# Kernel tuning notes

Hardware: AMD Instinct MI355X
Metric: run time of the kernel (lower is better)

Reference implementation:

```python
import jax, jax.numpy as jnp
import numpy as np
from jax import lax

B, IN_C, H, W = 2, 256, 80, 80
OUT_C = 256
INTER = IN_C // 16          # 16
C4 = IN_C // 4              # 64
K = 3
DIL = [7, 5, 2, 1]
PADS = [(K + (K - 1) * (d - 1)) // 2 for d in DIL]  # same-padding per module formula


def conv2d(x, w, b=None, pad=0, dil=1, groups=1):
    out = lax.conv_general_dilated(
        x, w, (1, 1), [(pad, pad), (pad, pad)], rhs_dilation=(dil, dil),
        dimension_numbers=('NCHW', 'OIHW', 'NCHW'), feature_group_count=groups)
    if b is not None:
        out = out + b[None, :, None, None]
    return out


def bnorm(x, g, b, eps=1e-3):
    # BatchNorm2d in training mode (fresh module): biased batch stats, eps=0.001
    m = x.mean((0, 2, 3), keepdims=True)
    v = x.var((0, 2, 3), keepdims=True)
    return (x - m) * lax.rsqrt(v + eps) * g[None, :, None, None] + b[None, :, None, None]


def gnorm(x, g, b, groups=4, eps=1e-5):
    Bb, C, Hh, Ww = x.shape
    xr = x.reshape(Bb, groups, C // groups, Hh, Ww)
    m = xr.mean((2, 3, 4), keepdims=True)
    v = xr.var((2, 3, 4), keepdims=True)
    xr = (xr - m) * lax.rsqrt(v + eps)
    return xr.reshape(Bb, C, Hh, Ww) * g[None, :, None, None] + b[None, :, None, None]


def setup_inputs() -> dict:
    keys = jax.random.split(jax.random.key(0), 40)

    def w_init(k, shape):
        fan = float(np.prod(shape[1:]))
        return jax.random.normal(k, shape, jnp.float32) / np.sqrt(fan)

    d = {}
    d['z'] = jax.random.normal(keys[0], (B, IN_C, H, W), jnp.float32)
    for i in range(4):  # depthwise dilated convs: (C4, 1, 3, 3)
        d[f'w_at{i}'] = w_init(keys[1 + 2 * i], (C4, 1, K, K))
        d[f'b_at{i}'] = jax.random.normal(keys[2 + 2 * i], (C4,), jnp.float32) * 0.02
    d['gn_w'] = 1.0 + 0.05 * jax.random.normal(keys[9], (IN_C,), jnp.float32)
    d['gn_b'] = 0.05 * jax.random.normal(keys[10], (IN_C,), jnp.float32)
    d['conv_w'] = w_init(keys[11], (IN_C, IN_C, 1, 1))
    d['conv_b'] = jax.random.normal(keys[12], (IN_C,), jnp.float32) * 0.02
    d['c5a_w'] = w_init(keys[13], (INTER, IN_C, 3, 3))
    d['bn5a_w'] = 1.0 + 0.05 * jax.random.normal(keys[14], (INTER,), jnp.float32)
    d['bn5a_b'] = 0.05 * jax.random.normal(keys[15], (INTER,), jnp.float32)
    d['c5c_w'] = w_init(keys[16], (INTER, IN_C, 3, 3))
    d['bn5c_w'] = 1.0 + 0.05 * jax.random.normal(keys[17], (INTER,), jnp.float32)
    d['bn5c_b'] = 0.05 * jax.random.normal(keys[18], (INTER,), jnp.float32)
    d['pq_w'] = w_init(keys[19], (INTER // 8, INTER, 1, 1))
    d['pq_b'] = jax.random.normal(keys[20], (INTER // 8,), jnp.float32) * 0.02
    d['pk_w'] = w_init(keys[21], (INTER // 8, INTER, 1, 1))
    d['pk_b'] = jax.random.normal(keys[22], (INTER // 8,), jnp.float32) * 0.02
    d['pv_w'] = w_init(keys[23], (INTER, INTER, 1, 1))
    d['pv_b'] = jax.random.normal(keys[24], (INTER,), jnp.float32) * 0.02
    d['pa_gamma'] = 0.5 * jnp.ones((1,), jnp.float32)  # nonzero so attn path is exercised
    d['ca_gamma'] = 0.5 * jnp.ones((1,), jnp.float32)
    d['c5b_w'] = w_init(keys[25], (INTER, INTER, 3, 3))
    d['bn5b_w'] = 1.0 + 0.05 * jax.random.normal(keys[26], (INTER,), jnp.float32)
    d['bn5b_b'] = 0.05 * jax.random.normal(keys[27], (INTER,), jnp.float32)
    d['c5d_w'] = w_init(keys[28], (INTER, INTER, 3, 3))
    d['bn5d_w'] = 1.0 + 0.05 * jax.random.normal(keys[29], (INTER,), jnp.float32)
    d['bn5d_b'] = 0.05 * jax.random.normal(keys[30], (INTER,), jnp.float32)
    d['c6_w'] = w_init(keys[31], (OUT_C, INTER, 1, 1))
    d['c6_b'] = jax.random.normal(keys[32], (OUT_C,), jnp.float32) * 0.02
    return d


def reference(z, w_at0, b_at0, w_at1, b_at1, w_at2, b_at2, w_at3, b_at3,
              gn_w, gn_b, conv_w, conv_b,
              c5a_w, bn5a_w, bn5a_b, c5c_w, bn5c_w, bn5c_b,
              pq_w, pq_b, pk_w, pk_b, pv_w, pv_b, pa_gamma, ca_gamma,
              c5b_w, bn5b_w, bn5b_b, c5d_w, bn5d_w, bn5d_b, c6_w, c6_b):
    parts = jnp.split(z, 4, axis=1)
    ws = [w_at0, w_at1, w_at2, w_at3]
    bs = [b_at0, b_at1, b_at2, b_at3]
    zs = [conv2d(parts[i], ws[i], bs[i], pad=PADS[i], dil=DIL[i], groups=C4)
          for i in range(4)]
    zc = jnp.concatenate(zs, axis=1)
    zc = jax.nn.gelu(conv2d(gnorm(zc, gn_w, gn_b), conv_w, conv_b), approximate=False)

    # --- DABlock ---
    feat1 = jax.nn.relu(bnorm(conv2d(zc, c5a_w, pad=1), bn5a_w, bn5a_b))
    Bb, C, Hh, Ww = feat1.shape
    N = Hh * Ww
    # PAM: full HWxHW attention
    q = conv2d(feat1, pq_w, pq_b).reshape(Bb, -1, N)   # (B, C//8, N)
    k = conv2d(feat1, pk_w, pk_b).reshape(Bb, -1, N)
    v = conv2d(feat1, pv_w, pv_b).reshape(Bb, C, N)
    energy = jnp.einsum('bcn,bcm->bnm', q, k)          # (B, N, N)
    att = jax.nn.softmax(energy, axis=-1)
    pa = jnp.einsum('bcm,bnm->bcn', v, att).reshape(Bb, C, Hh, Ww)
    pa = pa_gamma * pa + feat1
    pa_conv = jax.nn.relu(bnorm(conv2d(pa, c5b_w, pad=1), bn5b_w, bn5b_b))

    feat2 = jax.nn.relu(bnorm(conv2d(zc, c5c_w, pad=1), bn5c_w, bn5c_b))
    # CAM: CxC attention
    xf = feat2.reshape(Bb, C, N)
    e = jnp.einsum('bcn,bdn->bcd', xf, xf)             # (B, C, C)
    e = e.max(-1, keepdims=True) - e
    att_c = jax.nn.softmax(e, axis=-1)
    ca = jnp.einsum('bcd,bdn->bcn', att_c, xf).reshape(Bb, C, Hh, Ww)
    ca = ca_gamma * ca + feat2
    ca_conv = jax.nn.relu(bnorm(conv2d(ca, c5d_w, pad=1), bn5d_w, bn5d_b))

    # Dropout2d(p=0.05) is identity in eval mode
    out = jax.nn.relu(conv2d(pa_conv + ca_conv, c6_w, c6_b))
    return out
```

## Files before the change

kernel.cpp:

```cpp
#include <hip/hip_runtime.h>
#include <math.h>

#define HW 6400

typedef __attribute__((ext_vector_type(8))) short bf16x8;
typedef __attribute__((ext_vector_type(4))) float f32x4;

__device__ __forceinline__ float wredsum(float v){
  #pragma unroll
  for (int o = 32; o; o >>= 1) v += __shfl_xor(v, o);
  return v;
}

__device__ __forceinline__ unsigned short f2bf(float f){
  unsigned int u = __float_as_uint(f);
  u += 0x7FFF + ((u >> 16) & 1);
  return (unsigned short)(u >> 16);
}

__device__ __forceinline__ float bf2f(unsigned short s){
  return __uint_as_float((unsigned int)s << 16);
}

__device__ __forceinline__ unsigned int cvt_pk_bf16(float lo, float hi){
  unsigned int r;
  asm("v_cvt_pk_bf16_f32 %0, %1, %2" : "=v"(r) : "v"(lo), "v"(hi));
  return r;
}

__device__ __forceinline__ float gelu(float v){
  return 0.5f * v * (1.f + erff(v * 0.70710678118f));
}

__global__ __launch_bounds__(256) void k_prep(
    const float* __restrict__ wa, const float* __restrict__ wc,
    const float* __restrict__ wb, const float* __restrict__ wd,
    const float* __restrict__ cw, const float* __restrict__ gn_sc,
    const float* __restrict__ cb,
    unsigned short* __restrict__ wbbf,
    unsigned short* __restrict__ cwbf, float* __restrict__ cbp,
    unsigned short* __restrict__ wbbf2){
  int bx = blockIdx.x;
  int tid = threadIdx.x;
  if (bx < 288){
    int i = bx * 256 + tid;
    if (i < 73728){
      int j = i & 7, l = (i >> 3) & 63, f = (i >> 9) & 1, ss = i >> 10;
      int k = ss * 32 + (l >> 4) * 8 + j;
      int off = k >> 8, ic = k & 255;
      int oc = f * 16 + (l & 15);
      float v = (oc < 16) ? wa[(oc * 256 + ic) * 9 + off]
                          : wc[((oc - 16) * 256 + ic) * 9 + off];
      wbbf[i] = f2bf(v);
    }
  } else if (bx < 800){
    int i = (bx - 288) * 256 + tid;
    int b = i >> 16, r = i & 65535;
    int j = r & 7, l = (r >> 3) & 63, f = (r >> 9) & 15, ss = r >> 13;
    int ic = ss * 32 + (l >> 4) * 8 + j;
    int oc = f * 16 + (l & 15);
    cwbf[i] = f2bf(cw[oc * 256 + ic] * gn_sc[(b * 256 + ic) * 2]);
  } else if (bx < 832){
    int bb = bx - 800;
    int b = bb >> 4;
    int oc = (bb & 15) * 16 + (tid >> 4);
    int cp = tid & 15;
    float s2 = 0.f;
    #pragma unroll
    for (int k = 0; k < 16; k++){
      int c = cp * 16 + k;
      s2 += cw[oc * 256 + c] * gn_sc[(b * 256 + c) * 2 + 1];
    }
    s2 += __shfl_xor(s2, 1); s2 += __shfl_xor(s2, 2);
    s2 += __shfl_xor(s2, 4); s2 += __shfl_xor(s2, 8);
    if (cp == 0) cbp[b * 256 + oc] = cb[oc] + s2;
  } else {
    int i = (bx - 832) * 256 + tid;
    if (i < 9216){
      int j = i & 7, l = (i >> 3) & 63, f = (i >> 9) & 1, off = i >> 10;
      int kk = (l >> 4) * 8 + j;
      int oc = f * 16 + (l & 15);
      float v = 0.f;
      if (oc < 16 && kk < 16)        v = wb[(oc * 16 + kk) * 9 + off];
      else if (oc >= 16 && kk >= 16) v = wd[((oc - 16) * 16 + (kk - 16)) * 9 + off];
      wbbf2[i] = f2bf(v);
    }
  }
}

__global__ __launch_bounds__(256) void k_dwt(
    const float* __restrict__ z,
    const float* __restrict__ w0, const float* __restrict__ b0,
    const float* __restrict__ w1, const float* __restrict__ b1,
    const float* __restrict__ w2, const float* __restrict__ b2,
    const float* __restrict__ w3, const float* __restrict__ b3,
    unsigned short* __restrict__ zbf, float* __restrict__ gnpart){
  __shared__ unsigned short lt[64][66];
  int tid = threadIdx.x;
  int g = blockIdx.y, b = blockIdx.z;
  int p0 = blockIdx.x * 64;
  int lane = tid & 63, s = tid >> 6;
  int pix = p0 + lane;
  int h = pix / 80, w = pix % 80;
  const float* wp; const float* bp; int d;
  if (g == 0){ wp = w0; bp = b0; d = 7; }
  else if (g == 1){ wp = w1; bp = b1; d = 5; }
  else if (g == 2){ wp = w2; bp = b2; d = 2; }
  else            { wp = w3; bp = b3; d = 1; }
  int offr[9]; float msk[9];
  #pragma unroll
  for (int kh = 0; kh < 3; kh++){
    #pragma unroll
    for (int kw = 0; kw < 3; kw++){
      bool ok = ((unsigned)(h + (kh - 1) * d) < 80u) && ((unsigned)(w + (kw - 1) * d) < 80u);
      offr[kh * 3 + kw] = ok ? ((kh - 1) * d * 80 + (kw - 1) * d) : 0;
      msk[kh * 3 + kw] = ok ? 1.f : 0.f;
    }
  }
  const float* zb = z + (size_t)(b * 256 + g * 64) * HW + pix;
  for (int j = 0; j < 16; j++){
    int cl = s * 16 + j;
    const float* zin = zb + (size_t)cl * HW;
    const float* wr = wp + cl * 9;
    float acc = bp[cl];
    #pragma unroll
    for (int k = 0; k < 9; k++) acc = fmaf(wr[k], zin[offr[k]] * msk[k], acc);
    float S = wredsum(acc), Q = wredsum(acc * acc);
    if (lane == 0){
      int cg = b * 256 + g * 64 + cl;
      gnpart[(cg * 100 + blockIdx.x) * 2]     = S;
      gnpart[(cg * 100 + blockIdx.x) * 2 + 1] = Q;
    }
    lt[lane][cl] = f2bf(acc);
  }
  __syncthreads();
  int pr = tid >> 2, q = tid & 3;
  const unsigned short* src = &lt[pr][q * 16];
  unsigned int tmp[8];
  #pragma unroll
  for (int u = 0; u < 8; u++) tmp[u] = *(const unsigned int*)(src + u * 2);
  uint4 v0 = make_uint4(tmp[0], tmp[1], tmp[2], tmp[3]);
  uint4 v1 = make_uint4(tmp[4], tmp[5], tmp[6], tmp[7]);
  unsigned short* dst = zbf + ((size_t)b * HW + p0 + pr) * 256 + g * 64 + q * 16;
  *(uint4*)dst = v0;
  *(uint4*)(dst + 8) = v1;
}

__global__ __launch_bounds__(256) void k_gnfin(
    const float* __restrict__ gnpart, const float* __restrict__ gn_w,
    const float* __restrict__ gn_b, float* __restrict__ gn_sc){
  int tid = threadIdx.x; int bg = blockIdx.x;
  int b = bg >> 2, g = bg & 3;
  size_t base = (size_t)(b * 256 + g * 64) * 200;
  float S = 0.f, Q = 0.f;
  for (int i = tid; i < 6400; i += 256){
    S += gnpart[base + 2 * i];
    Q += gnpart[base + 2 * i + 1];
  }
  S = wredsum(S); Q = wredsum(Q);
  __shared__ float l[8];
  int lane = tid & 63, wid = tid >> 6;
  if (lane == 0){ l[wid] = S; l[4 + wid] = Q; }
  __syncthreads();
  float SS = l[0] + l[1] + l[2] + l[3];
  float QQ = l[4] + l[5] + l[6] + l[7];
  float M = 64.f * HW;
  float mean = SS / M;
  float var = QQ / M - mean * mean;
  float rstd = rsqrtf(var + 1e-5f);
  if (tid < 64){
    int c = g * 64 + tid;
    float sc = gn_w[c] * rstd;
    float sh = gn_b[c] - mean * sc;
    gn_sc[(b * 256 + c) * 2] = sc;
    gn_sc[(b * 256 + c) * 2 + 1] = sh;
  }
}

__global__ __launch_bounds__(256) void k_conv1_mfma(
    const unsigned short* __restrict__ zbf,
    const unsigned short* __restrict__ cwbf,
    const float* __restrict__ cbp,
    unsigned short* __restrict__ zbfT){
  __shared__ __align__(16) unsigned char lmem[64 * 512];
  unsigned short* lda = (unsigned short*)lmem;
  unsigned short* lout = (unsigned short*)lmem;
  int tid = threadIdx.x;
  int p0 = blockIdx.x * 64, ocg = blockIdx.y, b = blockIdx.z;
  #pragma unroll
  for (int k = 0; k < 8; k++){
    int m = tid + k * 256;
    int i = m >> 5, c = m & 31;
    bf16x8 val = *(const bf16x8*)(zbf + ((size_t)b * HW + p0 + i) * 256 + c * 8);
    *(bf16x8*)(lda + i * 256 + (c ^ (i & 7)) * 8) = val;
  }
  __syncthreads();
  int wv = tid >> 6, l = tid & 63;
  int row = l & 15, kg = l >> 4;
  int i = wv * 16 + row;
  f32x4 acc0 = {0.f,0.f,0.f,0.f}, acc1 = {0.f,0.f,0.f,0.f};
  f32x4 acc2 = {0.f,0.f,0.f,0.f}, acc3 = {0.f,0.f,0.f,0.f};
  const unsigned short* wp = cwbf + (size_t)b * 65536 + (ocg * 4) * 512 + l * 8;
  #pragma unroll
  for (int s = 0; s < 8; s++){
    int c = s * 4 + kg;
    bf16x8 a = *(const bf16x8*)(lda + i * 256 + (c ^ (i & 7)) * 8);
    const unsigned short* wps = wp + s * 8192;
    bf16x8 b0 = *(const bf16x8*)(wps);
    bf16x8 b1 = *(const bf16x8*)(wps + 512);
    bf16x8 b2 = *(const bf16x8*)(wps + 1024);
    bf16x8 b3 = *(const bf16x8*)(wps + 1536);
    acc0 = __builtin_amdgcn_mfma_f32_16x16x32_bf16(a, b0, acc0, 0, 0, 0);
    acc1 = __builtin_amdgcn_mfma_f32_16x16x32_bf16(a, b1, acc1, 0, 0, 0);
    acc2 = __builtin_amdgcn_mfma_f32_16x16x32_bf16(a, b2, acc2, 0, 0, 0);
    acc3 = __builtin_amdgcn_mfma_f32_16x16x32_bf16(a, b3, acc3, 0, 0, 0);
  }
  __syncthreads();
  const float* cbb = cbp + b * 256 + ocg * 64;
  int oc_l = l & 15;
  int pl = wv * 16 + kg * 4;
  float bs0 = cbb[oc_l], bs1 = cbb[16 + oc_l], bs2 = cbb[32 + oc_l], bs3 = cbb[48 + oc_l];
  #pragma unroll
  for (int r = 0; r < 4; r++){
    lout[(pl + r) * 72 + oc_l]      = f2bf(gelu(acc0[r] + bs0));
    lout[(pl + r) * 72 + 16 + oc_l] = f2bf(gelu(acc1[r] + bs1));
    lout[(pl + r) * 72 + 32 + oc_l] = f2bf(gelu(acc2[r] + bs2));
    lout[(pl + r) * 72 + 48 + oc_l] = f2bf(gelu(acc3[r] + bs3));
  }
  __syncthreads();
  int pix = tid >> 2, q = tid & 3;
  unsigned short* dst = zbfT + ((size_t)b * HW + p0 + pix) * 256 + ocg * 64 + q * 16;
  const unsigned short* src = lout + pix * 72 + q * 16;
  *(uint4*)dst       = *(const uint4*)src;
  *(uint4*)(dst + 8) = *(const uint4*)(src + 8);
}

__device__ __forceinline__ void c5_gload(bf16x8* r, const unsigned short* zbase,
    int p0, int irow, int c31, const int* hh, const int* ww, int off){
  int dy = off / 3 - 1, dx = off % 3 - 1;
  int doff = dy * 80 + dx;
  #pragma unroll
  for (int k = 0; k < 8; k++){
    int op = p0 + irow + k * 8;
    bool v = ((unsigned)(hh[k] + dy) < 80u) && ((unsigned)(ww[k] + dx) < 80u);
    int sp = v ? (op + doff) : op;
    bf16x8 val = *(const bf16x8*)(zbase + (size_t)sp * 256 + c31 * 8);
    if (!v) val = (bf16x8){0, 0, 0, 0, 0, 0, 0, 0};
    r[k] = val;
  }
}

__global__ __launch_bounds__(256) void k_conv5ac2(
    const unsigned short* __restrict__ zbfT,
    const unsigned short* __restrict__ wbbf,
    float* __restrict__ fpre, float* __restrict__ bnpart){
  __shared__ __align__(16) unsigned short lda[64 * 256];
  int tid = threadIdx.x;
  int och = blockIdx.y, b = blockIdx.z;
  int p0 = blockIdx.x * 64;
  int irow = tid >> 5, c31 = tid & 31;
  int hh[8], ww[8];
  #pragma unroll
  for (int k = 0; k < 8; k++){
    int op = p0 + irow + k * 8;
    hh[k] = op / 80; ww[k] = op % 80;
  }
  const unsigned short* zbase = zbfT + (size_t)b * HW * 256;
  bf16x8 r[8];
  c5_gload(r, zbase, p0, irow, c31, hh, ww, 0);
  #pragma unroll
  for (int k = 0; k < 8; k++){
    int i = irow + k * 8;
    *(bf16x8*)(lda + i * 256 + (c31 ^ (i & 7)) * 8) = r[k];
  }
  c5_gload(r, zbase, p0, irow, c31, hh, ww, 1);
  int wv = tid >> 6, l = tid & 63;
  int lrow = l & 15, kg = l >> 4;
  int li = wv * 16 + lrow;
  f32x4 acc = {0.f, 0.f, 0.f, 0.f};
  for (int off = 0; off < 9; off++){
    __syncthreads();
    const unsigned short* wp = wbbf + (size_t)off * 8192 + och * 512 + l * 8;
    #pragma unroll
    for (int s = 0; s < 8; s++){
      int cc = s * 4 + kg;
      bf16x8 a = *(const bf16x8*)(lda + li * 256 + (cc ^ (li & 7)) * 8);
      bf16x8 bb = *(const bf16x8*)(wp + s * 1024);
      acc = __builtin_amdgcn_mfma_f32_16x16x32_bf16(a, bb, acc, 0, 0, 0);
    }
    if (off + 1 < 9){
      __syncthreads();
      #pragma unroll
      for (int k = 0; k < 8; k++){
        int i = irow + k * 8;
        *(bf16x8*)(lda + i * 256 + (c31 ^ (i & 7)) * 8) = r[k];
      }
      if (off + 2 < 9) c5_gload(r, zbase, p0, irow, c31, hh, ww, off + 2);
    }
  }
  __syncthreads();
  float* lout = (float*)lda;
  int ocl = l & 15;
  int pl = wv * 16 + kg * 4;
  #pragma unroll
  for (int rr = 0; rr < 4; rr++) lout[ocl * 68 + pl + rr] = acc[rr];
  __syncthreads();
  int oc = tid >> 4, px = (tid & 15) * 4;
  float4 v = *(float4*)(lout + oc * 68 + px);
  *(float4*)(fpre + ((size_t)(b * 32 + och * 16 + oc)) * HW + p0 + px) = v;
  float S = v.x + v.y + v.z + v.w;
  float Q = v.x * v.x + v.y * v.y + v.z * v.z + v.w * v.w;
  #pragma unroll
  for (int o2 = 1; o2 < 16; o2 <<= 1){ S += __shfl_xor(S, o2); Q += __shfl_xor(Q, o2); }
  if ((tid & 15) == 0){
    int ocg = och * 16 + oc;
    bnpart[ocg * 400 + (b * 100 + blockIdx.x) * 2]     = S;
    bnpart[ocg * 400 + (b * 100 + blockIdx.x) * 2 + 1] = Q;
  }
}

__global__ __launch_bounds__(256) void k_featqkv(
    const float* __restrict__ fpre, const float* __restrict__ bnpart,
    const float* __restrict__ w1, const float* __restrict__ b1,
    const float* __restrict__ w2, const float* __restrict__ b2,
    const float* __restrict__ pqw, const float* __restrict__ pqb,
    const float* __restrict__ pkw, const float* __restrict__ pkb,
    const float* __restrict__ pvw, const float* __restrict__ pvb,
    float* __restrict__ feat, float* __restrict__ qkvT){
  __shared__ float lS[8][32], lQ[8][32], lsc[64];
  int tid = threadIdx.x; int b = blockIdx.y;
  {
    int oc = tid & 31, sl = tid >> 5;
    float S = 0.f, Q = 0.f;
    for (int i = sl; i < 200; i += 8){
      S += bnpart[oc * 400 + i * 2];
      Q += bnpart[oc * 400 + i * 2 + 1];
    }
    lS[sl][oc] = S; lQ[sl][oc] = Q;
    __syncthreads();
    if (tid < 32){
      float SS = 0.f, QQ = 0.f;
      #pragma unroll
      for (int s = 0; s < 8; s++){ SS += lS[s][tid]; QQ += lQ[s][tid]; }
      float M = 2.f * HW;
      float mean = SS / M, var = QQ / M - mean * mean;
      float rstd = rsqrtf(var + 1e-3f);
      float w  = (tid < 16) ? w1[tid] : w2[tid - 16];
      float bb = (tid < 16) ? b1[tid] : b2[tid - 16];
      float sc = w * rstd;
      lsc[tid * 2] = sc; lsc[tid * 2 + 1] = bb - mean * sc;
    }
    __syncthreads();
  }
  int n = blockIdx.x * 256 + tid;
  float f1[16], f2[16];
  #pragma unroll
  for (int c = 0; c < 16; c++){
    float v1 = fpre[(b * 32 + c) * HW + n] * lsc[c * 2] + lsc[c * 2 + 1];
    f1[c] = fmaxf(v1, 0.f);
    float v2 = fpre[(b * 32 + 16 + c) * HW + n] * lsc[(16 + c) * 2] + lsc[(16 + c) * 2 + 1];
    f2[c] = fmaxf(v2, 0.f);
    feat[(b * 32 + c) * HW + n] = f1[c];
    feat[(b * 32 + 16 + c) * HW + n] = f2[c];
  }
  float* o = qkvT + ((size_t)b * HW + n) * 20;
  #pragma unroll
  for (int j = 0; j < 2; j++){
    float q = pqb[j], k = pkb[j];
    #pragma unroll
    for (int c = 0; c < 16; c++){ q += pqw[j * 16 + c] * f1[c]; k += pkw[j * 16 + c] * f1[c]; }
    o[j] = q; o[2 + j] = k;
  }
  #pragma unroll
  for (int j = 0; j < 16; j++){
    float v = pvb[j];
    #pragma unroll
    for (int c = 0; c < 16; c++) v += pvw[j * 16 + c] * f1[c];
    o[4 + j] = v;
  }
}

__global__ __launch_bounds__(256) void k_pam_a(
    const float* __restrict__ qkvT, float* __restrict__ part){
  __shared__ __align__(16) float lk0[800];
  __shared__ __align__(16) float lk1[800];
  __shared__ __align__(16) unsigned short lvb[16][808];
  __shared__ float lred[4];
  int tid = threadIdx.x;
  int mc = blockIdx.y, b = blockIdx.z;
  float sqm = 0.f;
  for (int m = tid; m < 800; m += 256){
    const float* kv = qkvT + ((size_t)b * HW + mc * 800 + m) * 20;
    float4 a0 = *(const float4*)kv;
    lk0[m] = a0.z; lk1[m] = a0.w;
    sqm = fmaxf(sqm, a0.z * a0.z + a0.w * a0.w);
    float4 v0 = *(const float4*)(kv + 4);
    float4 v1 = *(const float4*)(kv + 8);
    float4 v2 = *(const float4*)(kv + 12);
    float4 v3 = *(const float4*)(kv + 16);
    lvb[0][m]  = f2bf(v0.x); lvb[1][m]  = f2bf(v0.y);
    lvb[2][m]  = f2bf(v0.z); lvb[3][m]  = f2bf(v0.w);
    lvb[4][m]  = f2bf(v1.x); lvb[5][m]  = f2bf(v1.y);
    lvb[6][m]  = f2bf(v1.z); lvb[7][m]  = f2bf(v1.w);
    lvb[8][m]  = f2bf(v2.x); lvb[9][m]  = f2bf(v2.y);
    lvb[10][m] = f2bf(v2.z); lvb[11][m] = f2bf(v2.w);
    lvb[12][m] = f2bf(v3.x); lvb[13][m] = f2bf(v3.y);
    lvb[14][m] = f2bf(v3.z); lvb[15][m] = f2bf(v3.w);
  }
  #pragma unroll
  for (int o = 32; o; o >>= 1) sqm = fmaxf(sqm, __shfl_xor(sqm, o));
  int lane = tid & 63, wid = tid >> 6;
  if (lane == 0) lred[wid] = sqm;
  __syncthreads();
  float kmax = sqrtf(fmaxf(fmaxf(lred[0], lred[1]), fmaxf(lred[2], lred[3])));
  int wv = tid >> 6, l = tid & 63;
  int row = l & 15, kg = l >> 4;
  int n = blockIdx.x * 64 + wv * 16 + row;
  const float* qp = qkvT + ((size_t)b * HW + n) * 20;
  float q0 = qp[0], q1 = qp[1];
  float mxr = sqrtf(q0 * q0 + q1 * q1) * kmax;
  f32x4 acc = {0.f, 0.f, 0.f, 0.f};
  float zp = 0.f;
  for (int t = 0; t < 25; t++){
    int m0 = t * 32 + kg * 8;
    float4 k0a = *(const float4*)&lk0[m0];
    float4 k0b = *(const float4*)&lk0[m0 + 4];
    float4 k1a = *(const float4*)&lk1[m0];
    float4 k1b = *(const float4*)&lk1[m0 + 4];
    float p0 = __expf(fmaf(q0, k0a.x, q1 * k1a.x) - mxr);
    float p1 = __expf(fmaf(q0, k0a.y, q1 * k1a.y) - mxr);
    float p2 = __expf(fmaf(q0, k0a.z, q1 * k1a.z) - mxr);
    float p3 = __expf(fmaf(q0, k0a.w, q1 * k1a.w) - mxr);
    float p4 = __expf(fmaf(q0, k0b.x, q1 * k1b.x) - mxr);
    float p5 = __expf(fmaf(q0, k0b.y, q1 * k1b.y) - mxr);
    float p6 = __expf(fmaf(q0, k0b.z, q1 * k1b.z) - mxr);
    float p7 = __expf(fmaf(q0, k0b.w, q1 * k1b.w) - mxr);
    zp += ((p0 + p1) + (p2 + p3)) + ((p4 + p5) + (p6 + p7));
    union { unsigned int u[4]; bf16x8 v; } pk;
    pk.u[0] = cvt_pk_bf16(p0, p1);
    pk.u[1] = cvt_pk_bf16(p2, p3);
    pk.u[2] = cvt_pk_bf16(p4, p5);
    pk.u[3] = cvt_pk_bf16(p6, p7);
    bf16x8 vb = *(const bf16x8*)&lvb[row][m0];
    acc = __builtin_amdgcn_mfma_f32_16x16x32_bf16(pk.v, vb, acc, 0, 0, 0);
  }
  zp += __shfl_xor(zp, 16);
  zp += __shfl_xor(zp, 32);
  float* pp = part + ((size_t)(b * 8 + mc) * 18) * HW;
  if (kg == 0){ pp[n] = mxr; pp[HW + n] = zp; }
  int c = l & 15;
  int nr = blockIdx.x * 64 + wv * 16 + (l >> 4) * 4;
  *(f32x4*)&pp[(size_t)(2 + c) * HW + nr] = acc;
}

__global__ __launch_bounds__(256) void k_cam_gram(
    const float* __restrict__ feat, float* __restrict__ e){
  int tid = threadIdx.x;
  int dd = blockIdx.x, c = blockIdx.y, b = blockIdx.z;
  const float* fc = feat + (b * 32 + 16 + c) * HW;
  const float* fd = feat + (b * 32 + 16 + dd) * HW;
  float S = 0.f;
  for (int i = tid; i < HW; i += 256) S += fc[i] * fd[i];
  S = wredsum(S);
  __shared__ float l[4];
  int lane = tid & 63, wid = tid >> 6;
  if (lane == 0) l[wid] = S;
  __syncthreads();
  if (tid == 0) e[(b * 16 + c) * 16 + dd] = l[0] + l[1] + l[2] + l[3];
}

__global__ __launch_bounds__(256) void k_merge(
    const float* __restrict__ part, const float* __restrict__ feat,
    const float* __restrict__ cam_e,
    const float* __restrict__ pa_g, const float* __restrict__ ca_g,
    unsigned short* __restrict__ mc){
  __shared__ float lsm[16][16];
  int tid = threadIdx.x; int b = blockIdx.y;
  if (tid < 16){
    const float* rowe = cam_e + (b * 16 + tid) * 16;
    float rr[16]; float mn = 1e30f;
    #pragma unroll
    for (int d = 0; d < 16; d++){ rr[d] = rowe[d]; mn = fminf(mn, rr[d]); }
    float p[16]; float s = 0.f;
    #pragma unroll
    for (int d = 0; d < 16; d++){ p[d] = __expf(mn - rr[d]); s += p[d]; }
    float inv = ca_g[0] / s;
    #pragma unroll
    for (int d = 0; d < 16; d++) lsm[tid][d] = p[d] * inv;
  }
  __syncthreads();
  int n = blockIdx.x * 256 + tid;
  float f1[16], f2[16];
  #pragma unroll
  for (int c = 0; c < 16; c++){
    f1[c] = feat[(b * 32 + c) * HW + n];
    f2[c] = feat[(b * 32 + 16 + c) * HW + n];
  }
  float mxs[8]; float mx = -1e30f;
  #pragma unroll
  for (int m8 = 0; m8 < 8; m8++){
    mxs[m8] = part[((size_t)(b * 8 + m8) * 18) * HW + n];
    mx = fmaxf(mx, mxs[m8]);
  }
  float Z = 0.f, a[16];
  #pragma unroll
  for (int c = 0; c < 16; c++) a[c] = 0.f;
  #pragma unroll
  for (int m8 = 0; m8 < 8; m8++){
    const float* pp = part + ((size_t)(b * 8 + m8) * 18) * HW + n;
    float r = __expf(mxs[m8] - mx);
    Z += pp[HW] * r;
    #pragma unroll
    for (int c = 0; c < 16; c++) a[c] += pp[(size_t)(2 + c) * HW] * r;
  }
  float invp = pa_g[0] / Z;
  union { unsigned short s[32]; uint4 u[4]; } rowo;
  #pragma unroll
  for (int c = 0; c < 16; c++)
    rowo.s[c] = f2bf(fmaf(a[c], invp, f1[c]));
  #pragma unroll
  for (int c = 0; c < 16; c++){
    float s = 0.f;
    #pragma unroll
    for (int d = 0; d < 16; d++) s = fmaf(lsm[c][d], f2[d], s);
    rowo.s[16 + c] = f2bf(s + f2[c]);
  }
  unsigned short* dst = mc + ((size_t)b * HW + n) * 32;
  *(uint4*)dst        = rowo.u[0];
  *(uint4*)(dst + 8)  = rowo.u[1];
  *(uint4*)(dst + 16) = rowo.u[2];
  *(uint4*)(dst + 24) = rowo.u[3];
}

__global__ __launch_bounds__(256) void k_conv5bd_mfma(
    const unsigned short* __restrict__ mc,
    const unsigned short* __restrict__ wbbf2,
    unsigned short* __restrict__ bdb, float* __restrict__ bnpart){
  __shared__ __align__(16) unsigned short lda[9 * 2048];
  __shared__ float lS[8][32], lQ[8][32];
  int tid = threadIdx.x;
  int b = blockIdx.z;
  int p0 = blockIdx.x * 64;
  int i = tid >> 2, q = tid & 3;
  int op = p0 + i;
  int h = op / 80, w = op % 80;
  const unsigned short* mb = mc + (size_t)b * HW * 32;
  #pragma unroll
  for (int off = 0; off < 9; off++){
    int dy = off / 3 - 1, dx = off % 3 - 1;
    bool v = ((unsigned)(h + dy) < 80u) && ((unsigned)(w + dx) < 80u);
    int sp = v ? (op + dy * 80 + dx) : op;
    bf16x8 val = *(const bf16x8*)(mb + (size_t)sp * 32 + q * 8);
    if (!v) val = (bf16x8){0, 0, 0, 0, 0, 0, 0, 0};
    int c8 = ((i & 1) * 4 + q) ^ ((i >> 1) & 7);
    *(bf16x8*)(lda + off * 2048 + (i >> 1) * 64 + c8 * 8) = val;
  }
  __syncthreads();
  int wv = tid >> 6, l = tid & 63;
  int row = l & 15, kg = l >> 4;
  int i2 = wv * 16 + row;
  f32x4 acc0 = {0.f, 0.f, 0.f, 0.f};
  f32x4 acc1 = {0.f, 0.f, 0.f, 0.f};
  #pragma unroll
  for (int off = 0; off < 9; off++){
    int c8 = ((i2 & 1) * 4 + kg) ^ ((i2 >> 1) & 7);
    bf16x8 a = *(const bf16x8*)(lda + off * 2048 + (i2 >> 1) * 64 + c8 * 8);
    bf16x8 b0 = *(const bf16x8*)(wbbf2 + off * 1024 + l * 8);
    bf16x8 b1 = *(const bf16x8*)(wbbf2 + off * 1024 + 512 + l * 8);
    acc0 = __builtin_amdgcn_mfma_f32_16x16x32_bf16(a, b0, acc0, 0, 0, 0);
    acc1 = __builtin_amdgcn_mfma_f32_16x16x32_bf16(a, b1, acc1, 0, 0, 0);
  }
  __syncthreads();
  float* lout = (float*)lda;
  int ocl = l & 15;
  int pl = wv * 16 + kg * 4;
  #pragma unroll
  for (int r = 0; r < 4; r++){
    lout[(pl + r) * 34 + ocl]      = acc0[r];
    lout[(pl + r) * 34 + 16 + ocl] = acc1[r];
  }
  __syncthreads();
  {
    int pix = tid >> 2, qq = tid & 3;
    const float* src = lout + pix * 34 + qq * 8;
    union { unsigned int u[4]; bf16x8 v; } pk;
    pk.u[0] = cvt_pk_bf16(src[0], src[1]);
    pk.u[1] = cvt_pk_bf16(src[2], src[3]);
    pk.u[2] = cvt_pk_bf16(src[4], src[5]);
    pk.u[3] = cvt_pk_bf16(src[6], src[7]);
    *(bf16x8*)(bdb + ((size_t)b * HW + p0 + pix) * 32 + qq * 8) = pk.v;
  }
  {
    int oc = tid & 31, grp = tid >> 5;
    float S = 0.f, Q = 0.f;
    #pragma unroll
    for (int r = 0; r < 8; r++){
      float v = lout[(grp * 8 + r) * 34 + oc];
      S += v; Q += v * v;
    }
    lS[grp][oc] = S; lQ[grp][oc] = Q;
  }
  __syncthreads();
  if (tid < 32){
    float S = 0.f, Q = 0.f;
    #pragma unroll
    for (int g2 = 0; g2 < 8; g2++){ S += lS[g2][tid]; Q += lQ[g2][tid]; }
    bnpart[tid * 400 + (b * 100 + blockIdx.x) * 2]     = S;
    bnpart[tid * 400 + (b * 100 + blockIdx.x) * 2 + 1] = Q;
  }
}

__global__ __launch_bounds__(256) void k_c6(
    const unsigned short* __restrict__ bdb, const float* __restrict__ bnpart,
    const float* __restrict__ w1, const float* __restrict__ b1,
    const float* __restrict__ w2, const float* __restrict__ b2,
    const float* __restrict__ w6, const float* __restrict__ b6,
    float* __restrict__ out){
  __shared__ float lS[8][32], lQ[8][32], lsc[64];
  int tid = threadIdx.x; int og = blockIdx.y * 32, b = blockIdx.z;
  {
    int oc = tid & 31, sl = tid >> 5;
    float S = 0.f, Q = 0.f;
    for (int i = sl; i < 200; i += 8){
      S += bnpart[oc * 400 + i * 2];
      Q += bnpart[oc * 400 + i * 2 + 1];
    }
    lS[sl][oc] = S; lQ[sl][oc] = Q;
    __syncthreads();
    if (tid < 32){
      float SS = 0.f, QQ = 0.f;
      #pragma unroll
      for (int s = 0; s < 8; s++){ SS += lS[s][tid]; QQ += lQ[s][tid]; }
      float M = 2.f * HW;
      float mean = SS / M, var = QQ / M - mean * mean;
      float rstd = rsqrtf(var + 1e-3f);
      float w  = (tid < 16) ? w1[tid] : w2[tid - 16];
      float bb = (tid < 16) ? b1[tid] : b2[tid - 16];
      float sc = w * rstd;
      lsc[tid * 2] = sc; lsc[tid * 2 + 1] = bb - mean * sc;
    }
    __syncthreads();
  }
  int n = blockIdx.x * 256 + tid;
  const unsigned short* rowp = bdb + ((size_t)b * HW + n) * 32;
  union { bf16x8 v[4]; unsigned short s[32]; } r;
  r.v[0] = *(const bf16x8*)(rowp);
  r.v[1] = *(const bf16x8*)(rowp + 8);
  r.v[2] = *(const bf16x8*)(rowp + 16);
  r.v[3] = *(const bf16x8*)(rowp + 24);
  float x[16];
  #pragma unroll
  for (int c = 0; c < 16; c++){
    float v1 = bf2f((unsigned short)r.s[c]) * lsc[c * 2] + lsc[c * 2 + 1];
    float v2 = bf2f((unsigned short)r.s[16 + c]) * lsc[(16 + c) * 2] + lsc[(16 + c) * 2 + 1];
    x[c] = fmaxf(v1, 0.f) + fmaxf(v2, 0.f);
  }
  #pragma unroll
  for (int o = 0; o < 32; o++){
    float a = b6[og + o];
    #pragma unroll
    for (int c = 0; c < 16; c++) a += w6[(og + o) * 16 + c] * x[c];
    out[(b * 256 + og + o) * HW + n] = fmaxf(a, 0.f);
  }
}

extern "C" void kernel_launch(void* const* d_in, const int* in_sizes, int n_in,
                              void* d_out, int out_size, void* d_ws, size_t ws_size,
                              hipStream_t stream){
  const float* z      = (const float*)d_in[0];
  const float* w_at0  = (const float*)d_in[1];
  const float* b_at0  = (const float*)d_in[2];
  const float* w_at1  = (const float*)d_in[3];
  const float* b_at1  = (const float*)d_in[4];
  const float* w_at2  = (const float*)d_in[5];
  const float* b_at2  = (const float*)d_in[6];
  const float* w_at3  = (const float*)d_in[7];
  const float* b_at3  = (const float*)d_in[8];
  const float* gn_w   = (const float*)d_in[9];
  const float* gn_b   = (const float*)d_in[10];
  const float* conv_w = (const float*)d_in[11];
  const float* conv_b = (const float*)d_in[12];
  const float* c5a_w  = (const float*)d_in[13];
  const float* bn5a_w = (const float*)d_in[14];
  const float* bn5a_b = (const float*)d_in[15];
  const float* c5c_w  = (const float*)d_in[16];
  const float* bn5c_w = (const float*)d_in[17];
  const float* bn5c_b = (const float*)d_in[18];
  const float* pq_w   = (const float*)d_in[19];
  const float* pq_b   = (const float*)d_in[20];
  const float* pk_w   = (const float*)d_in[21];
  const float* pk_b   = (const float*)d_in[22];
  const float* pv_w   = (const float*)d_in[23];
  const float* pv_b   = (const float*)d_in[24];
  const float* pa_g   = (const float*)d_in[25];
  const float* ca_g   = (const float*)d_in[26];
  const float* c5b_w  = (const float*)d_in[27];
  const float* bn5b_w = (const float*)d_in[28];
  const float* bn5b_b = (const float*)d_in[29];
  const float* c5d_w  = (const float*)d_in[30];
  const float* bn5d_w = (const float*)d_in[31];
  const float* bn5d_b = (const float*)d_in[32];
  const float* c6_w   = (const float*)d_in[33];
  const float* c6_b   = (const float*)d_in[34];

  float* ws = (float*)d_ws;
  unsigned short* ZBF    = (unsigned short*)ws;
  unsigned short* ZC2BFT = (unsigned short*)(ws + 1638400);
  unsigned short* CWBF   = (unsigned short*)(ws + 3276800);
  float* CBP     = ws + 3407872;
  float* FPRE    = ws + 3408384;
  float* FEAT    = FPRE + 409600;
  float* QKVT    = FEAT + 409600;
  unsigned short* MC  = (unsigned short*)(QKVT + 256000);
  unsigned short* BDB = (unsigned short*)(QKVT + 256000 + 204800);
  float* ST      = QKVT + 256000 + 409600;
  float* GN_SC    = ST;
  float* CAM_E    = ST + 1024;
  float* GN_PART  = ST + 2176;
  float* BNA_PART = ST + 104576;
  float* BNB_PART = ST + 117376;
  unsigned short* WBBF  = (unsigned short*)(ST + 130176);
  unsigned short* WBBF2 = (unsigned short*)(ST + 167040);
  float* PART = ws;

  k_dwt<<<dim3(100, 4, 2), 256, 0, stream>>>(z, w_at0, b_at0, w_at1, b_at1,
                                             w_at2, b_at2, w_at3, b_at3, ZBF, GN_PART);
  k_gnfin<<<8, 256, 0, stream>>>(GN_PART, gn_w, gn_b, GN_SC);
  k_prep<<<868, 256, 0, stream>>>(c5a_w, c5c_w, c5b_w, c5d_w, conv_w, GN_SC, conv_b,
                                  WBBF, CWBF, CBP, WBBF2);
  k_conv1_mfma<<<dim3(100, 4, 2), 256, 0, stream>>>(ZBF, CWBF, CBP, ZC2BFT);
  k_conv5ac2<<<dim3(100, 2, 2), 256, 0, stream>>>(ZC2BFT, WBBF, FPRE, BNA_PART);
  k_featqkv<<<dim3(25, 2), 256, 0, stream>>>(FPRE, BNA_PART, bn5a_w, bn5a_b,
                                             bn5c_w, bn5c_b, pq_w, pq_b, pk_w, pk_b,
                                             pv_w, pv_b, FEAT, QKVT);
  k_pam_a<<<dim3(100, 8, 2), 256, 0, stream>>>(QKVT, PART);
  k_cam_gram<<<dim3(16, 16, 2), 256, 0, stream>>>(FEAT, CAM_E);
  k_merge<<<dim3(25, 2), 256, 0, stream>>>(PART, FEAT, CAM_E, pa_g, ca_g, MC);
  k_conv5bd_mfma<<<dim3(100, 1, 2), 256, 0, stream>>>(MC, WBBF2, BDB, BNB_PART);
  k_c6<<<dim3(25, 8, 2), 256, 0, stream>>>(BDB, BNB_PART, bn5b_w, bn5b_b,
                                           bn5d_w, bn5d_b, c6_w, c6_b, (float*)d_out);
}
```

Baseline: 153.7 us.

## Double-buffer conv5ac LDS tile and widen merge and c6 grids

The conv5a/c kernel gets two LDS buffers so the next tap's tile can be written while the current one is read, which removes one barrier per tap. The merge kernel is split across four y-blocks (two for the PAM half, two for the CAM half, eight channels each) instead of one block computing all 32 channels. The c6 kernel handles 16 output channels per block instead of 32, so its grid doubles. Together these raise block counts on small, under-filled launches, at the cost of doubled LDS in conv5ac and redundant softmax-max and BN-stat work per block.

```diff
diff --git a/kernel.cpp b/kernel.cpp
--- a/kernel.cpp
+++ b/kernel.cpp
@@ -254,7 +254,7 @@
     const unsigned short* __restrict__ zbfT,
     const unsigned short* __restrict__ wbbf,
     float* __restrict__ fpre, float* __restrict__ bnpart){
-  __shared__ __align__(16) unsigned short lda[64 * 256];
+  __shared__ __align__(16) unsigned short lda[2][64 * 256];
   int tid = threadIdx.x;
   int och = blockIdx.y, b = blockIdx.z;
   int p0 = blockIdx.x * 64;
@@ -271,7 +271,7 @@
   #pragma unroll
   for (int k = 0; k < 8; k++){
     int i = irow + k * 8;
-    *(bf16x8*)(lda + i * 256 + (c31 ^ (i & 7)) * 8) = r[k];
+    *(bf16x8*)(lda[0] + i * 256 + (c31 ^ (i & 7)) * 8) = r[k];
   }
   c5_gload(r, zbase, p0, irow, c31, hh, ww, 1);
   int wv = tid >> 6, l = tid & 63;
@@ -280,20 +280,20 @@
   f32x4 acc = {0.f, 0.f, 0.f, 0.f};
   for (int off = 0; off < 9; off++){
     __syncthreads();
+    int buf = off & 1;
     const unsigned short* wp = wbbf + (size_t)off * 8192 + och * 512 + l * 8;
     #pragma unroll
     for (int s = 0; s < 8; s++){
       int cc = s * 4 + kg;
-      bf16x8 a = *(const bf16x8*)(lda + li * 256 + (cc ^ (li & 7)) * 8);
+      bf16x8 a = *(const bf16x8*)(lda[buf] + li * 256 + (cc ^ (li & 7)) * 8);
       bf16x8 bb = *(const bf16x8*)(wp + s * 1024);
       acc = __builtin_amdgcn_mfma_f32_16x16x32_bf16(a, bb, acc, 0, 0, 0);
     }
     if (off + 1 < 9){
-      __syncthreads();
       #pragma unroll
       for (int k = 0; k < 8; k++){
         int i = irow + k * 8;
-        *(bf16x8*)(lda + i * 256 + (c31 ^ (i & 7)) * 8) = r[k];
+        *(bf16x8*)(lda[buf ^ 1] + i * 256 + (c31 ^ (i & 7)) * 8) = r[k];
       }
       if (off + 2 < 9) c5_gload(r, zbase, p0, irow, c31, hh, ww, off + 2);
     }
@@ -474,62 +474,61 @@
     const float* __restrict__ cam_e,
     const float* __restrict__ pa_g, const float* __restrict__ ca_g,
     unsigned short* __restrict__ mc){
-  __shared__ float lsm[16][16];
-  int tid = threadIdx.x; int b = blockIdx.y;
-  if (tid < 16){
-    const float* rowe = cam_e + (b * 16 + tid) * 16;
-    float rr[16]; float mn = 1e30f;
-    #pragma unroll
-    for (int d = 0; d < 16; d++){ rr[d] = rowe[d]; mn = fminf(mn, rr[d]); }
-    float p[16]; float s = 0.f;
-    #pragma unroll
-    for (int d = 0; d < 16; d++){ p[d] = __expf(mn - rr[d]); s += p[d]; }
-    float inv = ca_g[0] / s;
-    #pragma unroll
-    for (int d = 0; d < 16; d++) lsm[tid][d] = p[d] * inv;
-  }
-  __syncthreads();
+  __shared__ float lsm[8][16];
+  int tid = threadIdx.x; int y = blockIdx.y, b = blockIdx.z;
   int n = blockIdx.x * 256 + tid;
-  float f1[16], f2[16];
-  #pragma unroll
-  for (int c = 0; c < 16; c++){
-    f1[c] = feat[(b * 32 + c) * HW + n];
-    f2[c] = feat[(b * 32 + 16 + c) * HW + n];
-  }
-  float mxs[8]; float mx = -1e30f;
-  #pragma unroll
-  for (int m8 = 0; m8 < 8; m8++){
-    mxs[m8] = part[((size_t)(b * 8 + m8) * 18) * HW + n];
-    mx = fmaxf(mx, mxs[m8]);
-  }
-  float Z = 0.f, a[16];
-  #pragma unroll
-  for (int c = 0; c < 16; c++) a[c] = 0.f;
-  #pragma unroll
-  for (int m8 = 0; m8 < 8; m8++){
-    const float* pp = part + ((size_t)(b * 8 + m8) * 18) * HW + n;
-    float r = __expf(mxs[m8] - mx);
-    Z += pp[HW] * r;
-    #pragma unroll
-    for (int c = 0; c < 16; c++) a[c] += pp[(size_t)(2 + c) * HW] * r;
-  }
-  float invp = pa_g[0] / Z;
-  union { unsigned short s[32]; uint4 u[4]; } rowo;
-  #pragma unroll
-  for (int c = 0; c < 16; c++)
-    rowo.s[c] = f2bf(fmaf(a[c], invp, f1[c]));
-  #pragma unroll
-  for (int c = 0; c < 16; c++){
-    float s = 0.f;
-    #pragma unroll
-    for (int d = 0; d < 16; d++) s = fmaf(lsm[c][d], f2[d], s);
-    rowo.s[16 + c] = f2bf(s + f2[c]);
-  }
-  unsigned short* dst = mc + ((size_t)b * HW + n) * 32;
-  *(uint4*)dst        = rowo.u[0];
-  *(uint4*)(dst + 8)  = rowo.u[1];
-  *(uint4*)(dst + 16) = rowo.u[2];
-  *(uint4*)(dst + 24) = rowo.u[3];
+  union { unsigned short s[8]; uint4 u; } rowo;
+  if (y < 2){
+    int c0 = y * 8;
+    float mxs[8]; float mx = -1e30f;
+    #pragma unroll
+    for (int m8 = 0; m8 < 8; m8++){
+      mxs[m8] = part[((size_t)(b * 8 + m8) * 18) * HW + n];
+      mx = fmaxf(mx, mxs[m8]);
+    }
+    float Z = 0.f, a[8];
+    #pragma unroll
+    for (int j = 0; j < 8; j++) a[j] = 0.f;
+    #pragma unroll
+    for (int m8 = 0; m8 < 8; m8++){
+      const float* pp = part + ((size_t)(b * 8 + m8) * 18) * HW + n;
+      float r = __expf(mxs[m8] - mx);
+      Z += pp[HW] * r;
+      #pragma unroll
+      for (int j = 0; j < 8; j++) a[j] += pp[(size_t)(2 + c0 + j) * HW] * r;
+    }
+    float invp = pa_g[0] / Z;
+    #pragma unroll
+    for (int j = 0; j < 8; j++)
+      rowo.s[j] = f2bf(fmaf(a[j], invp, feat[(b * 32 + c0 + j) * HW + n]));
+    *(uint4*)(mc + ((size_t)b * HW + n) * 32 + c0) = rowo.u;
+  } else {
+    int c0 = (y - 2) * 8;
+    if (tid < 8){
+      const float* rowe = cam_e + (b * 16 + c0 + tid) * 16;
+      float rr[16]; float mn = 1e30f;
+      #pragma unroll
+      for (int d = 0; d < 16; d++){ rr[d] = rowe[d]; mn = fminf(mn, rr[d]); }
+      float p[16]; float s = 0.f;
+      #pragma unroll
+      for (int d = 0; d < 16; d++){ p[d] = __expf(mn - rr[d]); s += p[d]; }
+      float inv = ca_g[0] / s;
+      #pragma unroll
+      for (int d = 0; d < 16; d++) lsm[tid][d] = p[d] * inv;
+    }
+    __syncthreads();
+    float f2[16];
+    #pragma unroll
+    for (int c = 0; c < 16; c++) f2[c] = feat[(b * 32 + 16 + c) * HW + n];
+    #pragma unroll
+    for (int j = 0; j < 8; j++){
+      float s = 0.f;
+      #pragma unroll
+      for (int d = 0; d < 16; d++) s = fmaf(lsm[j][d], f2[d], s);
+      rowo.s[j] = f2bf(s + f2[c0 + j]);
+    }
+    *(uint4*)(mc + ((size_t)b * HW + n) * 32 + 16 + c0) = rowo.u;
+  }
 }
 
 __global__ __launch_bounds__(256) void k_conv5bd_mfma(
@@ -617,7 +616,7 @@
     const float* __restrict__ w6, const float* __restrict__ b6,
     float* __restrict__ out){
   __shared__ float lS[8][32], lQ[8][32], lsc[64];
-  int tid = threadIdx.x; int og = blockIdx.y * 32, b = blockIdx.z;
+  int tid = threadIdx.x; int og = blockIdx.y * 16, b = blockIdx.z;
   {
     int oc = tid & 31, sl = tid >> 5;
     float S = 0.f, Q = 0.f;
@@ -656,7 +655,7 @@
     x[c] = fmaxf(v1, 0.f) + fmaxf(v2, 0.f);
   }
   #pragma unroll
-  for (int o = 0; o < 32; o++){
+  for (int o = 0; o < 16; o++){
     float a = b6[og + o];
     #pragma unroll
     for (int c = 0; c < 16; c++) a += w6[(og + o) * 16 + c] * x[c];
@@ -735,8 +734,8 @@
                                              pv_w, pv_b, FEAT, QKVT);
   k_pam_a<<<dim3(100, 8, 2), 256, 0, stream>>>(QKVT, PART);
   k_cam_gram<<<dim3(16, 16, 2), 256, 0, stream>>>(FEAT, CAM_E);
-  k_merge<<<dim3(25, 2), 256, 0, stream>>>(PART, FEAT, CAM_E, pa_g, ca_g, MC);
+  k_merge<<<dim3(25, 4, 2), 256, 0, stream>>>(PART, FEAT, CAM_E, pa_g, ca_g, MC);
   k_conv5bd_mfma<<<dim3(100, 1, 2), 256, 0, stream>>>(MC, WBBF2, BDB, BNB_PART);
-  k_c6<<<dim3(25, 8, 2), 256, 0, stream>>>(BDB, BNB_PART, bn5b_w, bn5b_b,
-                                           bn5d_w, bn5d_b, c6_w, c6_b, (float*)d_out);
-}
+  k_c6<<<dim3(25, 16, 2), 256, 0, stream>>>(BDB, BNB_PART, bn5b_w, bn5b_b,
+                                            bn5d_w, bn5d_b, c6_w, c6_b, (float*)d_out);
+}
```

Result: faster. 135.6 us (-11.8%).
